# Performance work log

Hardware: AMD Instinct MI355X
Metric: run time of the kernel (lower is better)

## Reference

```python
import jax, jax.numpy as jnp
import numpy as np

NUM_CLASSES = 80
STRIDES = (8, 16, 32)


def bce_logits(x, t):
    # numerically stable BCEWithLogits, reduction='none'
    return jnp.maximum(x, 0.) - x * t + jnp.log1p(jnp.exp(-jnp.abs(x)))


def decode_level(feat, stride):
    # feat: [B, C, H, W] -> decoded [B, HW, C], grid x/y [HW], strides [HW]
    B, C, H, W = feat.shape
    out = feat.reshape(B, C, H * W).transpose(0, 2, 1)  # [B, HW, C]
    yv, xv = jnp.meshgrid(jnp.arange(H), jnp.arange(W), indexing='ij')
    grid = jnp.stack([xv, yv], axis=-1).reshape(-1, 2).astype(feat.dtype)  # [HW, 2]
    xy = (out[..., :2] + grid[None]) * stride
    wh = jnp.exp(out[..., 2:4]) * stride
    out = jnp.concatenate([xy, wh, out[..., 4:]], axis=-1)
    return out, grid[:, 0], grid[:, 1], jnp.full((H * W,), float(stride), feat.dtype)


def pairwise_iou_cxcywh(g, p):
    # g: [G,4] gt boxes, p: [A,4] pred boxes (cx,cy,w,h) -> [G,A]
    tl = jnp.maximum(g[:, None, :2] - g[:, None, 2:] * 0.5, p[None, :, :2] - p[None, :, 2:] * 0.5)
    br = jnp.minimum(g[:, None, :2] + g[:, None, 2:] * 0.5, p[None, :, :2] + p[None, :, 2:] * 0.5)
    area_g = g[:, 2] * g[:, 3]
    area_p = p[:, 2] * p[:, 3]
    en = jnp.all(tl < br, axis=-1)
    inter = jnp.prod(br - tl, axis=-1) * en
    return inter / (area_g[:, None] + area_p[None, :] - inter + 1e-16)


def simota_assign(gt_boxes, gt_cls, bbox_p, cls_p, obj_p, xc, yc, strides):
    # per-image SimOTA label assignment (masked, jit-friendly)
    # gt_boxes [G,4], gt_cls [G] int, bbox_p [A,4], cls_p [A,C], obj_p [A,1]
    G = gt_boxes.shape[0]
    A = bbox_p.shape[0]
    gl = gt_boxes[:, 0:1] - 0.5 * gt_boxes[:, 2:3]
    gr = gt_boxes[:, 0:1] + 0.5 * gt_boxes[:, 2:3]
    gt_ = gt_boxes[:, 1:2] - 0.5 * gt_boxes[:, 3:4]
    gb = gt_boxes[:, 1:2] + 0.5 * gt_boxes[:, 3:4]
    in_box = (xc[None] > gl) & (xc[None] < gr) & (yc[None] > gt_) & (yc[None] < gb)  # [G,A]
    r = 2.5 * strides[None]
    in_ctr = ((xc[None] > gt_boxes[:, 0:1] - r) & (xc[None] < gt_boxes[:, 0:1] + r)
              & (yc[None] > gt_boxes[:, 1:2] - r) & (yc[None] < gt_boxes[:, 1:2] + r))
    geom = in_box | in_ctr
    anchor_ok = jnp.any(geom, axis=0)        # fg_mask candidate anchors [A]
    in_both = in_box & in_ctr                # [G,A]

    ious = pairwise_iou_cxcywh(gt_boxes, bbox_p)            # [G,A]
    ious = jnp.where(anchor_ok[None], ious, 0.)
    iou_cost = -jnp.log(ious + 1e-8)

    eps = 1e-8
    p = jnp.sqrt(jax.nn.sigmoid(cls_p) * jax.nn.sigmoid(obj_p))  # [A,C]
    logp = jnp.log(p + eps)
    log1mp = jnp.log(1. - p + eps)
    base = -jnp.sum(log1mp, axis=-1)                              # [A]
    sel = (logp - log1mp)[:, gt_cls]                              # [A,G]
    cls_cost = base[None, :] - sel.T                              # [G,A] = BCE(p, onehot).sum(-1)

    cost = cls_cost + 3.0 * iou_cost + 100000.0 * (~in_both) + 1e9 * (~anchor_ok[None])

    n_cand = min(10, A)
    topk_ious = jax.lax.top_k(ious, n_cand)[0]                    # [G,10]
    dyn_k = jnp.maximum(jnp.sum(topk_ious, axis=1).astype(jnp.int32), 1)  # [G]
    rank = jnp.argsort(jnp.argsort(cost, axis=1), axis=1)         # rank of each anchor per gt
    matching = (rank < dyn_k[:, None]) & anchor_ok[None]          # [G,A] bool

    am = jnp.sum(matching, axis=0)                                # anchors matched to >1 gt
    argmin_g = jnp.argmin(cost, axis=0)                           # [A]
    best = jnp.arange(G)[:, None] == argmin_g[None]               # [G,A]
    matching = jnp.where(am[None] > 1, best, matching)

    fg = jnp.any(matching, axis=0)                                # [A]
    matched_gt = jnp.argmax(matching, axis=0)                     # [A]
    pred_iou = jnp.sum(matching * ious, axis=0)                   # [A]
    cls_t = jax.nn.one_hot(gt_cls[matched_gt], NUM_CLASSES, dtype=bbox_p.dtype) * pred_iou[:, None]
    reg_t = gt_boxes[matched_gt]                                  # [A,4]
    return fg, cls_t, reg_t


def iou_elem(p, t):
    # elementwise IoU between matched pred/target boxes (cxcywh), IOUloss 'iou'
    tl = jnp.maximum(p[..., :2] - p[..., 2:] * 0.5, t[..., :2] - t[..., 2:] * 0.5)
    br = jnp.minimum(p[..., :2] + p[..., 2:] * 0.5, t[..., :2] + t[..., 2:] * 0.5)
    ap = p[..., 2] * p[..., 3]
    ag = t[..., 2] * t[..., 3]
    en = jnp.all(tl < br, axis=-1).astype(p.dtype)
    ai = jnp.prod(br - tl, axis=-1) * en
    return ai / (ap + ag - ai + 1e-16)


def yolo_loss(feat8, feat16, feat32, labels):
    outs, xs, ys, ss = [], [], [], []
    for feat, s in zip((feat8, feat16, feat32), STRIDES):
        o, x, y, st = decode_level(feat, s)
        outs.append(o); xs.append(x); ys.append(y); ss.append(st)
    outputs = jnp.concatenate(outs, axis=1)            # [B, A, 5+C]
    x_shifts = jnp.concatenate(xs)
    y_shifts = jnp.concatenate(ys)
    strides = jnp.concatenate(ss)
    xc = (x_shifts + 0.5) * strides                    # anchor centers [A]
    yc = (y_shifts + 0.5) * strides

    bbox_preds = outputs[..., :4]
    obj_preds = outputs[..., 4]
    cls_preds = outputs[..., 5:5 + NUM_CLASSES]

    labels_sg = jax.lax.stop_gradient(labels)
    gt_boxes = labels_sg[..., :4]
    gt_cls = labels_sg[..., 4].astype(jnp.int32)

    # assignment is @torch.no_grad in the original -> stop_gradient on its inputs
    fg, cls_t, reg_t = jax.vmap(simota_assign, in_axes=(0, 0, 0, 0, 0, None, None, None))(
        gt_boxes, gt_cls,
        jax.lax.stop_gradient(bbox_preds),
        jax.lax.stop_gradient(cls_preds),
        jax.lax.stop_gradient(outputs[..., 4:5]),
        xc, yc, strides)

    fg_f = fg.astype(outputs.dtype)                    # [B, A]
    iou = iou_elem(bbox_preds, reg_t)                  # [B, A]
    loss_iou = jnp.sum(fg_f * (1. - iou ** 2))
    loss_obj = jnp.sum(bce_logits(obj_preds, fg_f))
    loss_cls = jnp.sum(fg_f[..., None] * bce_logits(cls_preds, cls_t))
    num_fg = jnp.maximum(jnp.sum(fg_f), 1.)
    loss = (5.0 * loss_iou + 0.1 * loss_obj + loss_cls) / num_fg
    return loss


def setup_inputs() -> dict:
    key = jax.random.key(0)
    k1, k2, k3, k4, k5, k6, k7 = jax.random.split(key, 7)
    B, G = 32, 30
    feat8 = jax.random.normal(k1, (B, 85, 80, 80), jnp.float32)
    feat16 = jax.random.normal(k2, (B, 85, 40, 40), jnp.float32)
    feat32 = jax.random.normal(k3, (B, 85, 20, 20), jnp.float32)
    cx = jax.random.uniform(k4, (B, G, 1), jnp.float32, 60., 580.)
    cy = jax.random.uniform(k5, (B, G, 1), jnp.float32, 60., 580.)
    wh = jax.random.uniform(k6, (B, G, 2), jnp.float32, 20., 150.)
    cls = jax.random.randint(k7, (B, G, 1), 0, NUM_CLASSES).astype(jnp.float32)
    labels = jnp.concatenate([cx, cy, wh, cls], axis=-1)   # [B, G, 5] = cx,cy,w,h,cls
    return {"feat8": feat8, "feat16": feat16, "feat32": feat32, "labels": labels}


def reference(feat8, feat16, feat32, labels):
    return yolo_loss(feat8, feat16, feat32, labels)
```

## Files before the change

kernel.cpp:

```cpp
#include <hip/hip_runtime.h>
#include <cstdint>
#include <cstddef>

#define NB 32
#define NG 30
#define NA 8400
#define NC 80
#define SELB 512
#define MGRIDX 33
#define NBLK (MGRIDX * NB)
#define CAP 80
#define DCAP 2304
#define NITER 17

typedef unsigned long long u64;

struct Params {
  const float* f8; const float* f16; const float* f32; const float* lab;
  float*    bbox;
  float*    objlog;
  float*    po;
  float*    base_;
  unsigned* gbits;
  unsigned* obits;
  unsigned* mmask;
  unsigned* cand;
  unsigned* ccount;
  unsigned* dcount;
  unsigned* dlist;
  float*    part;
  float*    out;
};

__device__ __forceinline__ float fsigm(float x) {
  return __fdividef(1.0f, 1.0f + __expf(-x));
}

__device__ __forceinline__ void anchor_geom(int a, int& x, int& y, int& W, int& hw,
                                            float& stride, int& lvl) {
  if (a < 6400)      { W = 80; hw = 6400; stride = 8.f;  lvl = 0; int i = a;        y = i / 80; x = i - y * 80; }
  else if (a < 8000) { W = 40; hw = 1600; stride = 16.f; lvl = 1; int i = a - 6400; y = i / 40; x = i - y * 40; }
  else               { W = 20; hw = 400;  stride = 32.f; lvl = 2; int i = a - 8000; y = i / 20; x = i - y * 20; }
}

__device__ __forceinline__ float pair_iou(float px, float py, float pw, float ph,
                                          float glx, float gty, float grx, float gby,
                                          float area_g) {
  float tlx = fmaxf(glx, px - pw * 0.5f);
  float tly = fmaxf(gty, py - ph * 0.5f);
  float brx = fminf(grx, px + pw * 0.5f);
  float bry = fminf(gby, py + ph * 0.5f);
  float inter = ((tlx < brx) && (tly < bry)) ? (brx - tlx) * (bry - tly) : 0.0f;
  return __fdividef(inter, area_g + pw * ph - inter + 1e-16f);
}

__device__ __forceinline__ float cost_of(float4 pb, float po, float bs, unsigned gb,
                                         int g, float glx, float gty, float grx,
                                         float gby, float area_g, float xl,
                                         float& iou_out) {
  bool ok = (gb >> 31) & 1u;
  float iou = pair_iou(pb.x, pb.y, pb.z, pb.w, glx, gty, grx, gby, area_g);
  iou = ok ? iou : 0.0f;
  float iou_cost = -__logf(iou + 1e-8f);
  float pc = fsigm(xl);
  float pr = sqrtf(pc * po);
  float cls_cost = bs - (__logf(pr + 1e-8f) - __logf(1.0f - pr + 1e-8f));
  float c = cls_cost + 3.0f * iou_cost;
  c = c + (((gb >> g) & 1u) ? 0.0f : 100000.0f);
  c = c + (ok ? 0.0f : 1000000000.0f);
  iou_out = iou;
  return c;
}

__device__ __forceinline__ u64 packkey(float c, int a) {
  unsigned b = __float_as_uint(c);
  b = (b & 0x80000000u) ? ~b : (b | 0x80000000u);
  return ((u64)b << 32) | (unsigned)a;
}

__device__ float base_of(const Params& p, int b, int a, float po) {
  int lvl = (a < 6400) ? 0 : (a < 8000) ? 1 : 2;
  int hw  = (lvl == 0) ? 6400 : (lvl == 1) ? 1600 : 400;
  int loff = (lvl == 0) ? 0 : (lvl == 1) ? 6400 : 8000;
  const float* f = (lvl == 0) ? p.f8 : (lvl == 1) ? p.f16 : p.f32;
  int cb = b * 85 * hw + 5 * hw + (a - loff);
  float bs = 0.0f;
#pragma unroll 1
  for (int c = 0; c < NC; c++) {
    float xl = f[cb + c * hw];
    float pc = fsigm(xl);
    float pr = sqrtf(pc * po);
    bs -= __logf(1.0f - pr + 1e-8f);
  }
  return bs;
}

__global__ __launch_bounds__(256) void k_zero(Params p) {
  int i = blockIdx.x * 256 + threadIdx.x;
  if (i < NB * NG + NB) p.ccount[i] = 0u;
}

__global__ __launch_bounds__(256) void k_stage(Params p) {
  __shared__ float sgt[NG * 5];
  int b = blockIdx.y;
  int tid = threadIdx.x;
  if (tid < NG * 5) sgt[tid] = p.lab[b * NG * 5 + tid];
  __syncthreads();
  int a = blockIdx.x * 256 + tid;
  if (a >= NA) return;
  p.mmask[b * NA + a] = 0u;

  int x, y, W, hw, lvl; float stride;
  anchor_geom(a, x, y, W, hw, stride, lvl);
  const float* f = (lvl == 0) ? p.f8 : (lvl == 1) ? p.f16 : p.f32;
  int loff = (lvl == 0) ? 0 : (lvl == 1) ? 6400 : 8000;
  int fb = b * 85 * hw + (a - loff);

  float tx = f[fb];
  float ty = f[fb + hw];
  float tw = f[fb + 2 * hw];
  float th = f[fb + 3 * hw];
  float ob = f[fb + 4 * hw];

  float px = (tx + (float)x) * stride;
  float py = (ty + (float)y) * stride;
  float pw = __expf(tw) * stride;
  float ph = __expf(th) * stride;
  ((float4*)p.bbox)[b * NA + a] = make_float4(px, py, pw, ph);
  p.objlog[b * NA + a] = ob;
  p.po[b * NA + a] = fsigm(ob);

  float xc = ((float)x + 0.5f) * stride;
  float yc = ((float)y + 0.5f) * stride;
  float r = 2.5f * stride;
  float plx = px - 0.5f * pw, prx = px + 0.5f * pw;
  float pty = py - 0.5f * ph, pby = py + 0.5f * ph;
  unsigned gb = 0, ov = 0; int ok = 0;
#pragma unroll
  for (int g = 0; g < NG; g++) {
    float gx = sgt[g * 5], gy = sgt[g * 5 + 1], gw = sgt[g * 5 + 2], gh = sgt[g * 5 + 3];
    float glx = gx - 0.5f * gw, grx = gx + 0.5f * gw;
    float gty_ = gy - 0.5f * gh, gby = gy + 0.5f * gh;
    bool inb = (xc > glx) && (xc < grx) && (yc > gty_) && (yc < gby);
    bool inc = (xc > gx - r) && (xc < gx + r) && (yc > gy - r) && (yc < gy + r);
    ok |= (inb || inc) ? 1 : 0;
    bool ib = inb && inc;
    gb |= (unsigned)ib << g;
    bool o = (fmaxf(glx, plx) < fminf(grx, prx)) && (fmaxf(gty_, pty) < fminf(gby, pby));
    ov |= (unsigned)o << g;
    if (ib) {
      unsigned slot = atomicAdd(&p.ccount[b * NG + g], 1u);
      if (slot < CAP) p.cand[(b * NG + g) * CAP + slot] = (unsigned)a;
    }
  }
  gb |= (unsigned)ok << 31;
  p.gbits[b * NA + a] = gb;
  p.obits[b * NA + a] = ok ? ov : 0u;
  if (gb & 0x3FFFFFFFu) {
    unsigned s = atomicAdd(&p.dcount[b], 1u);
    if (s < DCAP) p.dlist[b * DCAP + s] = (unsigned)a;
  }
}

__global__ __launch_bounds__(256) void k_base(Params p) {
  int b = blockIdx.y;
  unsigned n = p.dcount[b]; if (n > DCAP) n = DCAP;
  unsigned i = blockIdx.x * 256 + threadIdx.x;
  if (i >= n) return;
  int a = (int)p.dlist[b * DCAP + i];
  int lvl = (a < 6400) ? 0 : (a < 8000) ? 1 : 2;
  int hw  = (lvl == 0) ? 6400 : (lvl == 1) ? 1600 : 400;
  int loff = (lvl == 0) ? 0 : (lvl == 1) ? 6400 : 8000;
  const float* f = (lvl == 0) ? p.f8 : (lvl == 1) ? p.f16 : p.f32;
  int cb = b * 85 * hw + 5 * hw + (a - loff);
  float po = p.po[b * NA + a];
  float bs = 0.0f;
#pragma unroll 8
  for (int c = 0; c < NC; c++) {
    float xl = f[cb + c * hw];
    float pc = fsigm(xl);
    float pr = sqrtf(pc * po);
    bs -= __logf(1.0f - pr + 1e-8f);
  }
  p.base_[b * NA + a] = bs;
}

__device__ __forceinline__ u64 block_min_u64(u64 k, int tid, u64* swk) {
#pragma unroll
  for (int off = 32; off; off >>= 1) {
    u64 k2 = __shfl_down(k, off, 64);
    if (k2 < k) k = k2;
  }
  int wv = tid >> 6;
  if ((tid & 63) == 0) swk[wv] = k;
  __syncthreads();
  u64 m = swk[0];
#pragma unroll
  for (int w = 1; w < SELB / 64; w++) if (swk[w] < m) m = swk[w];
  __syncthreads();
  return m;
}

__global__ __launch_bounds__(SELB) void k_sel(Params p) {
  __shared__ float sh_iou[NA];
  __shared__ float swv[SELB / 64];
  __shared__ int   swi[SELB / 64];
  __shared__ u64   swk[SELB / 64];
  __shared__ int   sh_excl[10];
  __shared__ int   scnt;
  int bg = blockIdx.x;
  int b = bg / NG, g = bg % NG;
  int tid = threadIdx.x;
  if (tid == 0) scnt = 0;

  const float* gt = p.lab + (b * NG + g) * 5;
  float gx = gt[0], gy = gt[1], gw = gt[2], gh = gt[3];
  int cg = (int)gt[4];
  float glx = gx - 0.5f * gw, grx = gx + 0.5f * gw;
  float gty = gy - 0.5f * gh, gby = gy + 0.5f * gh;
  float area_g = gw * gh;
  const float4*   bb  = (const float4*)p.bbox + b * NA;
  const unsigned* obv = p.obits + b * NA;
  __syncthreads();

  unsigned obw[NITER];
#pragma unroll
  for (int it = 0; it < NITER; it++) {
    int a = it * SELB + tid;
    obw[it] = (a < NA) ? obv[a] : 0u;
  }
#pragma unroll
  for (int it = 0; it < NITER; it++) {
    int a = it * SELB + tid;
    bool act = (obw[it] >> g) & 1u;
    u64 bal = __ballot(act);
    if (bal) {
      int lane = tid & 63;
      int leader = __ffsll(bal) - 1;
      int basec = 0;
      if (lane == leader) basec = atomicAdd(&scnt, __popcll(bal));
      basec = __shfl(basec, leader, 64);
      if (act) {
        int pre = __popcll(bal & ((1ull << lane) - 1ull));
        float4 pb = bb[a];
        float iou = pair_iou(pb.x, pb.y, pb.z, pb.w, glx, gty, grx, gby, area_g);
        sh_iou[basec + pre] = iou;
      }
    }
  }
  __syncthreads();
  int n = scnt;

  float sum = 0.0f;
  for (int rnd = 0; rnd < 10; rnd++) {
    float mv = -1.0f; int mi = -1;
    for (int j = tid; j < n; j += SELB) {
      float v = sh_iou[j];
      if (v > mv) { mv = v; mi = j; }
    }
#pragma unroll
    for (int off = 32; off; off >>= 1) {
      float v2 = __shfl_down(mv, off, 64);
      int   i2 = __shfl_down(mi, off, 64);
      if (v2 > mv) { mv = v2; mi = i2; }
    }
    if ((tid & 63) == 0) { swv[tid >> 6] = mv; swi[tid >> 6] = mi; }
    __syncthreads();
    float bv = swv[0]; int bi = swi[0];
#pragma unroll
    for (int w = 1; w < SELB / 64; w++)
      if (swv[w] > bv) { bv = swv[w]; bi = swi[w]; }
    sum += fmaxf(bv, 0.0f);
    if (tid == 0 && bi >= 0) sh_iou[bi] = -1.0f;
    __syncthreads();
  }
  int dynk = (int)sum;
  if (dynk < 1) dynk = 1;

  unsigned nc = p.ccount[b * NG + g]; if (nc > CAP) nc = CAP;
  u64 key = ~0ull;
  if (tid < (int)nc) {
    int a = (int)p.cand[(b * NG + g) * CAP + tid];
    float4 pb = bb[a];
    float po_ = p.po[b * NA + a];
    float bs_ = p.base_[b * NA + a];
    unsigned gb_ = p.gbits[b * NA + a];
    int lvl = (a < 6400) ? 0 : (a < 8000) ? 1 : 2;
    int hw  = (lvl == 0) ? 6400 : (lvl == 1) ? 1600 : 400;
    int loff = (lvl == 0) ? 0 : (lvl == 1) ? 6400 : 8000;
    const float* f = (lvl == 0) ? p.f8 : (lvl == 1) ? p.f16 : p.f32;
    float xl = f[b * 85 * hw + (5 + cg) * hw + (a - loff)];
    float iou_;
    float c = cost_of(pb, po_, bs_, gb_, g, glx, gty, grx, gby, area_g, xl, iou_);
    key = packkey(c, a);
  }
  unsigned* mrow = p.mmask + b * NA;
  unsigned gbit = 1u << g;
  int matched = 0;
  for (int it = 0; it < dynk; it++) {
    u64 win = block_min_u64(key, tid, swk);
    if (win == ~0ull) break;
    if (key == win) {
      atomicOr(&mrow[(unsigned)(win & 0xFFFFFFFFu)], gbit);
      key = ~0ull;
    }
    matched++;
  }

  if (matched < dynk) {
    const unsigned* gbv = p.gbits + b * NA;
    const float*    pov = p.po + b * NA;
    for (int it = matched; it < dynk; it++) {
      u64 best = ~0ull;
      for (int al = tid; al < NA; al += SELB) {
        unsigned gb = gbv[al];
        if (!(gb >> 31)) continue;
        if ((gb >> g) & 1u) continue;
        bool skip = false;
        for (int e = matched; e < it; e++) if (sh_excl[e] == al) skip = true;
        if (skip) continue;
        float po_ = pov[al];
        float bs = base_of(p, b, al, po_);
        int lvl = (al < 6400) ? 0 : (al < 8000) ? 1 : 2;
        int hw  = (lvl == 0) ? 6400 : (lvl == 1) ? 1600 : 400;
        int loff = (lvl == 0) ? 0 : (lvl == 1) ? 6400 : 8000;
        const float* f = (lvl == 0) ? p.f8 : (lvl == 1) ? p.f16 : p.f32;
        float xl = f[b * 85 * hw + (5 + cg) * hw + (al - loff)];
        float4 pb = bb[al];
        float iou_;
        float c = cost_of(pb, po_, bs, gb, g, glx, gty, grx, gby, area_g, xl, iou_);
        u64 nk = packkey(c, al);
        if (nk < best) best = nk;
      }
      u64 win = block_min_u64(best, tid, swk);
      if (win == ~0ull) break;
      int aw = (int)(win & 0xFFFFFFFFu);
      if (best == win) {
        atomicOr(&mrow[aw], gbit);
        p.base_[b * NA + aw] = base_of(p, b, aw, pov[aw]);
      }
      if (tid == 0) sh_excl[it] = aw;
      __syncthreads();
    }
  }
}

__device__ __forceinline__ float block_sum(float val, volatile float* sw) {
#pragma unroll
  for (int off = 32; off > 0; off >>= 1) val += __shfl_down(val, off, 64);
  int lane = threadIdx.x & 63, wv = threadIdx.x >> 6;
  __syncthreads();
  if (lane == 0) sw[wv] = val;
  __syncthreads();
  float r = 0.0f;
  if (threadIdx.x == 0) r = sw[0] + sw[1] + sw[2] + sw[3];
  return r;
}

__global__ __launch_bounds__(256) void k_match(Params p) {
  __shared__ float sred[4];
  int b = blockIdx.y;
  int tid = threadIdx.x;
  int lane = tid & 63;
  int a = blockIdx.x * 256 + tid;
  bool valid = a < NA;

  float l_iou = 0.0f, l_obj = 0.0f, l_cls = 0.0f, l_nfg = 0.0f;
  unsigned mask = 0; int am = 0;
  bool fg = false; float pred_iou = 0.0f; int cg_ = 0;

  if (valid) {
    mask = p.mmask[b * NA + a];
    am = __popc(mask);
    fg = (mask != 0u);
    float ol = p.objlog[b * NA + a];
    float tfg = fg ? 1.0f : 0.0f;
    l_obj = fmaxf(ol, 0.0f) - ol * tfg + __logf(1.0f + __expf(-fabsf(ol)));
  }

  unsigned long long amb = __ballot(valid && am > 1);
  while (amb) {
    int src = __ffsll(amb) - 1;
    amb &= amb - 1ull;
    int aa = __shfl(a, src, 64);
    float4 pb = ((const float4*)p.bbox)[b * NA + aa];
    float po_ = p.po[b * NA + aa];
    float bs_ = p.base_[b * NA + aa];
    unsigned gb_ = p.gbits[b * NA + aa];

    int lvl = (aa < 6400) ? 0 : (aa < 8000) ? 1 : 2;
    int hw  = (lvl == 0) ? 6400 : (lvl == 1) ? 1600 : 400;
    int loff = (lvl == 0) ? 0 : (lvl == 1) ? 6400 : 8000;
    const float* f = (lvl == 0) ? p.f8 : (lvl == 1) ? p.f16 : p.f32;
    int cb = b * 85 * hw + 5 * hw + (aa - loff);

    float c = 3.4e38f; int gg = 0x7FFFFFFF;
    if (lane < NG) {
      const float* gtg = p.lab + (b * NG + lane) * 5;
      float gx = gtg[0], gy = gtg[1], gw = gtg[2], gh = gtg[3];
      int cg = (int)gtg[4];
      float xl = f[cb + cg * hw];
      float iou_;
      c = cost_of(pb, po_, bs_, gb_, lane,
                  gx - 0.5f * gw, gy - 0.5f * gh,
                  gx + 0.5f * gw, gy + 0.5f * gh, gw * gh, xl, iou_);
      gg = lane;
    }
#pragma unroll
    for (int off = 32; off; off >>= 1) {
      float c2 = __shfl_down(c, off, 64);
      int   g2 = __shfl_down(gg, off, 64);
      if (c2 < c || (c2 == c && g2 < gg)) { c = c2; gg = g2; }
    }
    gg = __shfl(gg, 0, 64);
    if (lane == src) mask = 1u << gg;
  }

  if (valid && fg) {
    l_nfg = 1.0f;
    int mg = __ffs(mask) - 1;
    const float* gtm = p.lab + (b * NG + mg) * 5;
    float gx = gtm[0], gy = gtm[1], gw = gtm[2], gh = gtm[3];
    cg_ = (int)gtm[4];
    float4 pb = ((const float4*)p.bbox)[b * NA + a];
    float iou = pair_iou(pb.x, pb.y, pb.z, pb.w,
                         gx - 0.5f * gw, gy - 0.5f * gh,
                         gx + 0.5f * gw, gy + 0.5f * gh, gw * gh);
    pred_iou = iou;
    l_iou = 1.0f - iou * iou;
  }

  unsigned long long fgb = __ballot(valid && fg);
  while (fgb) {
    int src = __ffsll(fgb) - 1;
    fgb &= fgb - 1ull;
    int   aa   = __shfl(a, src, 64);
    float piou = __shfl(pred_iou, src, 64);
    int   ccg  = __shfl(cg_, src, 64);

    int lvl = (aa < 6400) ? 0 : (aa < 8000) ? 1 : 2;
    int hw  = (lvl == 0) ? 6400 : (lvl == 1) ? 1600 : 400;
    int loff = (lvl == 0) ? 0 : (lvl == 1) ? 6400 : 8000;
    const float* f = (lvl == 0) ? p.f8 : (lvl == 1) ? p.f16 : p.f32;
    int cb = b * 85 * hw + 5 * hw + (aa - loff);

    float part = 0.0f;
#pragma unroll
    for (int c0 = 0; c0 < NC; c0 += 64) {
      int c = c0 + lane;
      if (c < NC) {
        float xl = f[cb + c * hw];
        float t = (c == ccg) ? piou : 0.0f;
        part += fmaxf(xl, 0.0f) - xl * t + __logf(1.0f + __expf(-fabsf(xl)));
      }
    }
#pragma unroll
    for (int off = 32; off; off >>= 1) part += __shfl_down(part, off, 64);
    if (lane == 0) l_cls += part;
  }

  float s0 = block_sum(l_iou, sred);
  float s1 = block_sum(l_obj, sred);
  float s2 = block_sum(l_cls, sred);
  float s3 = block_sum(l_nfg, sred);
  if (tid == 0) {
    ((float4*)p.part)[b * MGRIDX + blockIdx.x] = make_float4(s0, s1, s2, s3);
  }
}

__global__ __launch_bounds__(256) void k_final(Params p) {
  __shared__ float sred[4];
  int tid = threadIdx.x;
  float s0 = 0.0f, s1 = 0.0f, s2 = 0.0f, s3 = 0.0f;
  for (int i = tid; i < NBLK; i += 256) {
    float4 v = ((const float4*)p.part)[i];
    s0 += v.x; s1 += v.y; s2 += v.z; s3 += v.w;
  }
  s0 = block_sum(s0, sred);
  s1 = block_sum(s1, sred);
  s2 = block_sum(s2, sred);
  s3 = block_sum(s3, sred);
  if (tid == 0) {
    p.out[0] = (5.0f * s0 + 0.1f * s1 + s2) / fmaxf(s3, 1.0f);
  }
}

extern "C" void kernel_launch(void* const* d_in, const int* in_sizes, int n_in,
                              void* d_out, int out_size, void* d_ws, size_t ws_size,
                              hipStream_t stream) {
  Params p;
  p.f8  = (const float*)d_in[0];
  p.f16 = (const float*)d_in[1];
  p.f32 = (const float*)d_in[2];
  p.lab = (const float*)d_in[3];

  float* w = (float*)d_ws;
  p.bbox   = w;              w += (size_t)NB * NA * 4;
  p.objlog = w;              w += (size_t)NB * NA;
  p.po     = w;              w += (size_t)NB * NA;
  p.base_  = w;              w += (size_t)NB * NA;
  p.gbits  = (unsigned*)w;   w += (size_t)NB * NA;
  p.obits  = (unsigned*)w;   w += (size_t)NB * NA;
  p.mmask  = (unsigned*)w;   w += (size_t)NB * NA;
  p.cand   = (unsigned*)w;   w += (size_t)NB * NG * CAP;
  p.ccount = (unsigned*)w;   w += (size_t)NB * NG;
  p.dcount = (unsigned*)w;   w += (size_t)NB;
  p.dlist  = (unsigned*)w;   w += (size_t)NB * DCAP;
  p.part   = w;              w += (size_t)NBLK * 4;
  p.out    = (float*)d_out;

  dim3 gd(MGRIDX, NB);
  k_zero <<<dim3(4), 256, 0, stream>>>(p);
  k_stage<<<gd, 256, 0, stream>>>(p);
  k_base <<<dim3(DCAP / 256, NB), 256, 0, stream>>>(p);
  k_sel  <<<NB * NG, SELB, 0, stream>>>(p);
  k_match<<<gd, 256, 0, stream>>>(p);
  k_final<<<1, 256, 0, stream>>>(p);
}
```

Baseline: 207.6 us.

## Build per-GT candidate lists in shared memory and wave-aggregate dlist atomics

Per-(image, GT) candidate lists are no longer built in k_stage with a global atomic per hit. k_sel now builds them itself by scanning the gbits bits during its existing obits pass, compacting into shared memory with wave-ballot atomics. The dlist append in k_stage also switches from per-thread global atomics to one atomic per wavefront. This cuts global atomic contention in k_stage at the cost of an extra gbits read per anchor in k_sel, and the unrolled register prefetch of obits is dropped.

```diff
diff --git a/kernel.cpp b/kernel.cpp
--- a/kernel.cpp
+++ b/kernel.cpp
@@ -9,7 +9,7 @@
 #define SELB 512
 #define MGRIDX 33
 #define NBLK (MGRIDX * NB)
-#define CAP 80
+#define LCAP 128
 #define DCAP 2304
 #define NITER 17
 
@@ -24,8 +24,6 @@
   unsigned* gbits;
   unsigned* obits;
   unsigned* mmask;
-  unsigned* cand;
-  unsigned* ccount;
   unsigned* dcount;
   unsigned* dlist;
   float*    part;
@@ -96,8 +94,8 @@
 }
 
 __global__ __launch_bounds__(256) void k_zero(Params p) {
-  int i = blockIdx.x * 256 + threadIdx.x;
-  if (i < NB * NG + NB) p.ccount[i] = 0u;
+  int i = threadIdx.x;
+  if (i < NB) p.dcount[i] = 0u;
 }
 
 __global__ __launch_bounds__(256) void k_stage(Params p) {
@@ -144,21 +142,26 @@
     bool inb = (xc > glx) && (xc < grx) && (yc > gty_) && (yc < gby);
     bool inc = (xc > gx - r) && (xc < gx + r) && (yc > gy - r) && (yc < gy + r);
     ok |= (inb || inc) ? 1 : 0;
-    bool ib = inb && inc;
-    gb |= (unsigned)ib << g;
+    gb |= (unsigned)(inb && inc) << g;
     bool o = (fmaxf(glx, plx) < fminf(grx, prx)) && (fmaxf(gty_, pty) < fminf(gby, pby));
     ov |= (unsigned)o << g;
-    if (ib) {
-      unsigned slot = atomicAdd(&p.ccount[b * NG + g], 1u);
-      if (slot < CAP) p.cand[(b * NG + g) * CAP + slot] = (unsigned)a;
-    }
   }
   gb |= (unsigned)ok << 31;
   p.gbits[b * NA + a] = gb;
   p.obits[b * NA + a] = ok ? ov : 0u;
-  if (gb & 0x3FFFFFFFu) {
-    unsigned s = atomicAdd(&p.dcount[b], 1u);
-    if (s < DCAP) p.dlist[b * DCAP + s] = (unsigned)a;
+
+  bool has = (gb & 0x3FFFFFFFu) != 0u;
+  u64 bal = __ballot(has);
+  if (bal) {
+    int lane = tid & 63;
+    int leader = __ffsll(bal) - 1;
+    unsigned basec = 0;
+    if (lane == leader) basec = atomicAdd(&p.dcount[b], (unsigned)__popcll(bal));
+    basec = __shfl(basec, leader, 64);
+    if (has) {
+      unsigned s = basec + (unsigned)__popcll(bal & ((1ull << lane) - 1ull));
+      if (s < DCAP) p.dlist[b * DCAP + s] = (unsigned)a;
+    }
   }
 }
 
@@ -203,15 +206,16 @@
 
 __global__ __launch_bounds__(SELB) void k_sel(Params p) {
   __shared__ float sh_iou[NA];
+  __shared__ unsigned sh_cand[LCAP];
   __shared__ float swv[SELB / 64];
   __shared__ int   swi[SELB / 64];
   __shared__ u64   swk[SELB / 64];
   __shared__ int   sh_excl[10];
-  __shared__ int   scnt;
+  __shared__ int   scnt, scand;
   int bg = blockIdx.x;
   int b = bg / NG, g = bg % NG;
   int tid = threadIdx.x;
-  if (tid == 0) scnt = 0;
+  if (tid == 0) { scnt = 0; scand = 0; }
 
   const float* gt = p.lab + (b * NG + g) * 5;
   float gx = gt[0], gy = gt[1], gw = gt[2], gh = gt[3];
@@ -221,21 +225,18 @@
   float area_g = gw * gh;
   const float4*   bb  = (const float4*)p.bbox + b * NA;
   const unsigned* obv = p.obits + b * NA;
-  __syncthreads();
-
-  unsigned obw[NITER];
-#pragma unroll
+  const unsigned* gbv = p.gbits + b * NA;
+  __syncthreads();
+
+  int lane = tid & 63;
   for (int it = 0; it < NITER; it++) {
     int a = it * SELB + tid;
-    obw[it] = (a < NA) ? obv[a] : 0u;
-  }
-#pragma unroll
-  for (int it = 0; it < NITER; it++) {
-    int a = it * SELB + tid;
-    bool act = (obw[it] >> g) & 1u;
+    unsigned ob = 0u, gbw = 0u;
+    if (a < NA) { ob = obv[a]; gbw = gbv[a]; }
+    bool act = (ob >> g) & 1u;
+    bool cnd = (gbw >> g) & 1u;
     u64 bal = __ballot(act);
     if (bal) {
-      int lane = tid & 63;
       int leader = __ffsll(bal) - 1;
       int basec = 0;
       if (lane == leader) basec = atomicAdd(&scnt, __popcll(bal));
@@ -247,6 +248,17 @@
         sh_iou[basec + pre] = iou;
       }
     }
+    u64 bc = __ballot(cnd);
+    if (bc) {
+      int leader = __ffsll(bc) - 1;
+      int basec = 0;
+      if (lane == leader) basec = atomicAdd(&scand, __popcll(bc));
+      basec = __shfl(basec, leader, 64);
+      if (cnd) {
+        int s = basec + __popcll(bc & ((1ull << lane) - 1ull));
+        if (s < LCAP) sh_cand[s] = (unsigned)a;
+      }
+    }
   }
   __syncthreads();
   int n = scnt;
@@ -277,14 +289,14 @@
   int dynk = (int)sum;
   if (dynk < 1) dynk = 1;
 
-  unsigned nc = p.ccount[b * NG + g]; if (nc > CAP) nc = CAP;
+  int nc = scand; if (nc > LCAP) nc = LCAP;
   u64 key = ~0ull;
-  if (tid < (int)nc) {
-    int a = (int)p.cand[(b * NG + g) * CAP + tid];
+  if (tid < nc) {
+    int a = (int)sh_cand[tid];
     float4 pb = bb[a];
     float po_ = p.po[b * NA + a];
     float bs_ = p.base_[b * NA + a];
-    unsigned gb_ = p.gbits[b * NA + a];
+    unsigned gb_ = gbv[a];
     int lvl = (a < 6400) ? 0 : (a < 8000) ? 1 : 2;
     int hw  = (lvl == 0) ? 6400 : (lvl == 1) ? 1600 : 400;
     int loff = (lvl == 0) ? 0 : (lvl == 1) ? 6400 : 8000;
@@ -308,8 +320,7 @@
   }
 
   if (matched < dynk) {
-    const unsigned* gbv = p.gbits + b * NA;
-    const float*    pov = p.po + b * NA;
+    const float* pov = p.po + b * NA;
     for (int it = matched; it < dynk; it++) {
       u64 best = ~0ull;
       for (int al = tid; al < NA; al += SELB) {
@@ -502,15 +513,13 @@
   p.gbits  = (unsigned*)w;   w += (size_t)NB * NA;
   p.obits  = (unsigned*)w;   w += (size_t)NB * NA;
   p.mmask  = (unsigned*)w;   w += (size_t)NB * NA;
-  p.cand   = (unsigned*)w;   w += (size_t)NB * NG * CAP;
-  p.ccount = (unsigned*)w;   w += (size_t)NB * NG;
   p.dcount = (unsigned*)w;   w += (size_t)NB;
   p.dlist  = (unsigned*)w;   w += (size_t)NB * DCAP;
   p.part   = w;              w += (size_t)NBLK * 4;
   p.out    = (float*)d_out;
 
   dim3 gd(MGRIDX, NB);
-  k_zero <<<dim3(4), 256, 0, stream>>>(p);
+  k_zero <<<1, 256, 0, stream>>>(p);
   k_stage<<<gd, 256, 0, stream>>>(p);
   k_base <<<dim3(DCAP / 256, NB), 256, 0, stream>>>(p);
   k_sel  <<<NB * NG, SELB, 0, stream>>>(p);
```

Result: no change. 204.1 us (-1.7%).
